# Kernel optimization log

Measured on AMD Instinct MI355X. Metric: run time of the kernel, lower is better.

## Reference

```python
import jax, jax.numpy as jnp
import numpy as np
import math

B, S, D, H, M = 2, 2048, 1024, 16, 64
HD = D // H  # head_dim = 64


def setup_inputs() -> dict:
    key = jax.random.key(0)
    ks = jax.random.split(key, 16)
    inp = {
        "query": jax.random.normal(ks[0], (B, S, D), jnp.float32),
        "key": jax.random.normal(ks[1], (B, S, D), jnp.float32),
        "value": jax.random.normal(ks[2], (B, S, D), jnp.float32),
        "mask": jax.random.randint(ks[3], (B, 1, 1, S), 0, 2, jnp.int32),
        "Wq": jax.random.normal(ks[4], (D, D), jnp.float32) * 0.02,
        "bq": jnp.zeros((D,), jnp.float32),
        "Wk": jax.random.normal(ks[5], (D, D), jnp.float32) * 0.02,
        "bk": jnp.zeros((D,), jnp.float32),
        "Wv": jax.random.normal(ks[6], (D, D), jnp.float32) * 0.02,
        "bv": jnp.zeros((D,), jnp.float32),
        "Wo": jax.random.normal(ks[7], (D, D), jnp.float32) * 0.02,
        "bo": jnp.zeros((D,), jnp.float32),
        "m_k": jax.random.normal(ks[8], (1, M, D), jnp.float32) * (1.0 / HD),
        "m_v": jax.random.normal(ks[9], (1, M, D), jnp.float32) * (1.0 / M),
    }
    return inp


def reference(query, key, value, mask, Wq, bq, Wk, bk, Wv, bv, Wo, bo, m_k, m_v):
    b, nq, d = query.shape
    nk = key.shape[1]
    h, hd, m = H, HD, M
    scale = math.sqrt(hd)

    Q = query @ Wq.T + bq                      # [b, nq, d]
    K = key @ Wk.T + bk                        # [b, nk, d]
    V = value @ Wv.T + bv                      # [b, nk, d]

    mk = scale * jnp.broadcast_to(m_k, (b, m, d))           # sqrt(head_dim)*m_k
    mv = math.sqrt(m) * jnp.broadcast_to(m_v, (b, m, d))    # sqrt(m)*m_v

    K = jnp.concatenate([K, mk], axis=1)       # [b, nk+m, d]
    V = jnp.concatenate([V, mv], axis=1)

    Qh = Q.reshape(b, nq, h, hd).transpose(0, 2, 1, 3)           # [b,h,nq,hd]
    Kh = K.reshape(b, nk + m, h, hd).transpose(0, 2, 1, 3)       # [b,h,nk+m,hd]
    Vh = V.reshape(b, nk + m, h, hd).transpose(0, 2, 1, 3)

    energy = jnp.einsum('bhqd,bhkd->bhqk', Qh, Kh) / scale       # [b,h,nq,nk+m]
    # mask only the first nk key columns; memory slots are never masked
    masked = jnp.where(mask == 0, jnp.float32(-1e20), energy[..., :nk])
    energy = jnp.concatenate([masked, energy[..., nk:]], axis=-1)

    attention = jax.nn.softmax(energy, axis=-1)
    x = jnp.einsum('bhqk,bhkd->bhqd', attention, Vh)             # [b,h,nq,hd]
    x = x.transpose(0, 2, 1, 3).reshape(b, nq, d)
    return x @ Wo.T + bo
```

## Files before the change

kernel.cpp:

```cpp
#include <hip/hip_runtime.h>
#include <hip/hip_bf16.h>
#include <stdint.h>

#define B_  2
#define S_  2048
#define D_  1024
#define H_  16
#define HD_ 64
#define M_  64
#define SKM (S_ + M_)
#define LOG2E 1.44269504088896340736f

typedef __attribute__((ext_vector_type(8))) short s16x8;
typedef __attribute__((ext_vector_type(4))) float f32x4;
typedef __attribute__((ext_vector_type(16))) float f32x16;

#define GLOAD16(gp, lp) __builtin_amdgcn_global_load_lds( \
    (const __attribute__((address_space(1))) void*)(gp),  \
    (__attribute__((address_space(3))) void*)(lp), 16, 0, 0)

#define WAITVM(N) do { asm volatile("s_waitcnt vmcnt(" #N ")" ::: "memory"); \
                       __builtin_amdgcn_sched_barrier(0); } while (0)
#define BARRIER() do { asm volatile("" ::: "memory"); \
                       __builtin_amdgcn_s_barrier(); \
                       asm volatile("" ::: "memory"); } while (0)

__device__ __forceinline__ unsigned short f2bf(float f) {
  union { float f; unsigned int u; } v; v.f = f;
  unsigned int r = v.u + 0x7fffu + ((v.u >> 16) & 1u);
  return (unsigned short)(r >> 16);
}

__device__ __forceinline__ unsigned pkbf(float lo, float hi) {
  union { __hip_bfloat162 b; unsigned u; } t;
  t.b = __float22bfloat162_rn(make_float2(lo, hi));
  return t.u;
}

__global__ void compact_mask(const int* __restrict__ mask,
                             int* __restrict__ idx, int* __restrict__ cnt) {
  const int b = blockIdx.x;
  __shared__ int base, wsum[4];
  if (threadIdx.x == 0) base = 0;
  const int lane = threadIdx.x & 63, w = threadIdx.x >> 6;
  __syncthreads();
  for (int c = 0; c < S_; c += 256) {
    int key = c + threadIdx.x;
    int mv = mask[b * S_ + key];
    unsigned long long bal = __ballot(mv != 0);
    int pre = __popcll(bal & ((1ull << lane) - 1ull));
    if (lane == 0) wsum[w] = __popcll(bal);
    __syncthreads();
    int woff = 0;
    for (int i = 0; i < w; i++) woff += wsum[i];
    int tot = wsum[0] + wsum[1] + wsum[2] + wsum[3];
    if (mv) idx[b * S_ + base + woff + pre] = key;
    __syncthreads();
    if (threadIdx.x == 0) base += tot;
    __syncthreads();
  }
  if (threadIdx.x == 0) cnt[b] = base;
}

__global__ void cvt_fused(const float* __restrict__ q,
                          const float* __restrict__ w0, const float* __restrict__ w1,
                          const float* __restrict__ w2, const float* __restrict__ w3,
                          const float* __restrict__ key, const float* __restrict__ value,
                          unsigned short* __restrict__ qf,
                          unsigned short* __restrict__ o0, unsigned short* __restrict__ o1,
                          unsigned short* __restrict__ o2, unsigned short* __restrict__ o3,
                          unsigned short* __restrict__ kf, unsigned short* __restrict__ vf,
                          const int* __restrict__ idx, const int* __restrict__ cnt) {
  const size_t NQs = (size_t)B_ * S_ * D_;
  if (blockIdx.x < 8192) {
    size_t i = ((size_t)blockIdx.x * 256 + threadIdx.x) * 4;
    const float* in; unsigned short* out; size_t off;
    if (i < NQs) { in = q; out = qf; off = i; }
    else {
      size_t j = i - NQs;
      int wsel = (int)(j >> 20);
      off = j & ((1u << 20) - 1);
      in  = (wsel == 0) ? w0 : (wsel == 1) ? w1 : (wsel == 2) ? w2 : w3;
      out = (wsel == 0) ? o0 : (wsel == 1) ? o1 : (wsel == 2) ? o2 : o3;
    }
    float4 v = *(const float4*)&in[off];
    ushort4 o;
    o.x = f2bf(v.x); o.y = f2bf(v.y); o.z = f2bf(v.z); o.w = f2bf(v.w);
    *(ushort4*)&out[off] = o;
  } else {
    int gid = blockIdx.x - 8192;
    int kv = gid >> 12, rem = gid & 4095;
    int b = rem >> 11, j = rem & 2047;
    if (j >= cnt[b]) return;
    const float* in = kv ? value : key;
    unsigned short* out = kv ? vf : kf;
    int src = idx[b * S_ + j];
    const float* ip = in + ((size_t)(b * S_) + src) * D_;
    unsigned short* op = out + ((size_t)(b * S_) + j) * D_;
    int t = threadIdx.x * 4;
    float4 v = *(const float4*)&ip[t];
    ushort4 o;
    o.x = f2bf(v.x); o.y = f2bf(v.y); o.z = f2bf(v.z); o.w = f2bf(v.w);
    *(ushort4*)&op[t] = o;
  }
}

__global__ void fill_mem(const float* __restrict__ mk, const float* __restrict__ mv,
                         unsigned short* __restrict__ Kb, unsigned short* __restrict__ VtG,
                         const int* __restrict__ cnt) {
  int i = blockIdx.x * 256 + threadIdx.x;
  int row = i >> 10, col = i & 1023;
  int hI = col >> 6, dd = col & 63;
  unsigned short kv = f2bf(8.0f * mk[i]);
  unsigned short vv = f2bf(8.0f * mv[i]);
#pragma unroll
  for (int b = 0; b < B_; b++) {
    int c = cnt[b];
    Kb[((size_t)(b * SKM) + c + row) * D_ + col] = kv;
    VtG[((size_t)(b * H_ + hI) * HD_ + dd) * SKM + c + row] = vv;
  }
}

__device__ __forceinline__ void gemm_core2(
    const unsigned short* __restrict__ A,
    const unsigned short* __restrict__ Bw,
    unsigned short* As, unsigned short* Bs,
    int mBase, int nBase, int K,
    int tid, f32x4 acc[4][2]) {
  const int lane = tid & 63, w = tid >> 6;
  const int wr = w >> 2, wc = w & 3;
  const int lr = lane & 15, lk = lane >> 4;
  const int srow = tid >> 2;
  const int cd = tid & 3;
  const int ca = cd ^ ((srow >> 1) & 3);
  const int NT = K / 32;

#define STAGE_(buf, k0)                                                          \
  {                                                                              \
    GLOAD16(&A[(size_t)(mBase + srow) * K + (k0) + ca * 8],                      \
            &As[(buf) * (128 * 32) + (w * 16) * 32]);                            \
    GLOAD16(&Bw[(size_t)(nBase + srow) * K + (k0) + ca * 8],                     \
            &Bs[(buf) * (128 * 32) + (w * 16) * 32]);                            \
  }

  STAGE_(0, 0);
  int cur = 0;
  for (int t = 0; t < NT; ++t) {
    if (t + 1 < NT) {
      STAGE_(cur ^ 1, (t + 1) * 32);
      WAITVM(2);
    } else {
      WAITVM(0);
    }
    BARRIER();
    s16x8 af[4], bf[2];
#pragma unroll
    for (int mi = 0; mi < 4; mi++) {
      int row = wr * 64 + mi * 16 + lr;
      af[mi] = *(const s16x8*)&As[cur * (128 * 32) + row * 32 + ((lk ^ ((row >> 1) & 3)) << 3)];
    }
#pragma unroll
    for (int ni = 0; ni < 2; ni++) {
      int row = wc * 32 + ni * 16 + lr;
      bf[ni] = *(const s16x8*)&Bs[cur * (128 * 32) + row * 32 + ((lk ^ ((row >> 1) & 3)) << 3)];
    }
#pragma unroll
    for (int mi = 0; mi < 4; mi++)
#pragma unroll
      for (int ni = 0; ni < 2; ni++)
        acc[mi][ni] = __builtin_amdgcn_mfma_f32_16x16x32_bf16(af[mi], bf[ni], acc[mi][ni], 0, 0, 0);
    BARRIER();
    cur ^= 1;
  }
#undef STAGE_
}

__global__ __launch_bounds__(512)
void gemm_qkv(const unsigned short* __restrict__ qf, const unsigned short* __restrict__ kf,
              const unsigned short* __restrict__ vf,
              const unsigned short* __restrict__ wq, const unsigned short* __restrict__ wk,
              const unsigned short* __restrict__ wv,
              const float* __restrict__ bq, const float* __restrict__ bk,
              const float* __restrict__ bv,
              unsigned short* __restrict__ Qb, unsigned short* __restrict__ Kb,
              unsigned short* __restrict__ Vt,
              const int* __restrict__ cnt) {
  __shared__ __align__(16) unsigned short As[2 * 128 * 32];
  __shared__ __align__(16) unsigned short Bs[2 * 128 * 32];
  const int z = blockIdx.x >> 8;
  const int local = blockIdx.x & 255;
  const int wsz = (local & 7) * 32 + (local >> 3);
  const int nBase = (wsz & 7) * 128, mBase = (wsz >> 3) * 128;
  const int bb = (mBase >= S_);
  if (z) {
    if (mBase - bb * S_ >= cnt[bb]) return;
  }
  const unsigned short* A  = (z == 0) ? qf : (z == 1) ? kf : vf;
  const unsigned short* Bw = (z == 0) ? wq : (z == 1) ? wk : wv;
  const float* bias        = (z == 0) ? bq : (z == 1) ? bk : bv;

  const int tid = threadIdx.x, lane = tid & 63;
  const int w = tid >> 6, wr = w >> 2, wc = w & 3;
  const int lr = lane & 15, lk = lane >> 4;

  const f32x4 fz = {0.f, 0.f, 0.f, 0.f};
  f32x4 acc[4][2];
#pragma unroll
  for (int i = 0; i < 4; i++)
#pragma unroll
    for (int j = 0; j < 2; j++) acc[i][j] = fz;

  gemm_core2(A, Bw, As, Bs, mBase, nBase, D_, tid, acc);

  const float alpha = (z == 0) ? 0.125f * LOG2E : 1.0f;
#pragma unroll
  for (int mi = 0; mi < 4; mi++)
#pragma unroll
    for (int ni = 0; ni < 2; ni++)
#pragma unroll
      for (int r = 0; r < 4; r++) {
        int gr = mBase + wr * 64 + mi * 16 + lk * 4 + r;
        int gc = nBase + wc * 32 + ni * 16 + lr;
        float v = (acc[mi][ni][r] + bias[gc]) * alpha;
        if (z == 2) {
          int s = gr - bb * S_;
          int hI = gc >> 6, dd = gc & 63;
          Vt[((size_t)(bb * H_ + hI) * HD_ + dd) * SKM + s] = f2bf(v);
        } else if (z == 1) {
          int orow = gr + bb * M_;
          Kb[(size_t)orow * D_ + gc] = f2bf(v);
        } else {
          Qb[(size_t)gr * D_ + gc] = f2bf(v);
        }
      }
}

__global__ __launch_bounds__(512)
void gemm_o(const unsigned short* __restrict__ A, const unsigned short* __restrict__ Bw,
            const float* __restrict__ bias, float* __restrict__ Cout) {
  __shared__ __align__(16) unsigned short As[2 * 128 * 32];
  __shared__ __align__(16) unsigned short Bs[2 * 128 * 32];
  const int local = blockIdx.x & 255;
  const int wsz = (local & 7) * 32 + (local >> 3);
  const int nBase = (wsz & 7) * 128, mBase = (wsz >> 3) * 128;
  const int tid = threadIdx.x, lane = tid & 63;
  const int w = tid >> 6, wr = w >> 2, wc = w & 3;
  const int lr = lane & 15, lk = lane >> 4;

  const f32x4 fz = {0.f, 0.f, 0.f, 0.f};
  f32x4 acc[4][2];
#pragma unroll
  for (int i = 0; i < 4; i++)
#pragma unroll
    for (int j = 0; j < 2; j++) acc[i][j] = fz;

  gemm_core2(A, Bw, As, Bs, mBase, nBase, D_, tid, acc);

#pragma unroll
  for (int mi = 0; mi < 4; mi++)
#pragma unroll
    for (int ni = 0; ni < 2; ni++)
#pragma unroll
      for (int r = 0; r < 4; r++) {
        int gr = mBase + wr * 64 + mi * 16 + lk * 4 + r;
        int gc = nBase + wc * 32 + ni * 16 + lr;
        Cout[(size_t)gr * D_ + gc] = acc[mi][ni][r] + bias[gc];
      }
}

__global__ __launch_bounds__(512)
void attn_kernel(const unsigned short* __restrict__ Qb,
                 const unsigned short* __restrict__ Kb,
                 const unsigned short* __restrict__ VtG,
                 const int* __restrict__ cnt,
                 unsigned short* __restrict__ Xb) {
  __shared__ __align__(16) unsigned short Ks[64 * 64];
  __shared__ __align__(16) unsigned short Vs[64 * 64];

  const int tid = threadIdx.x, lane = tid & 63, w = tid >> 6;
  const int l31 = lane & 31, hh = lane >> 5;
  const int qt = blockIdx.x, h = blockIdx.y, b = blockIdx.z;

  const int total = cnt[b] + M_;
  const int nt = (total + 63) >> 6;

  const int r0 = tid >> 3, c0 = tid & 7;
  const int ck = c0 ^ (r0 & 7);
  const unsigned short* Kg = Kb + (size_t)b * SKM * D_ + (size_t)h * HD_;
  const unsigned short* Vg = VtG + (size_t)(b * H_ + h) * HD_ * SKM;

  const unsigned short* qp = Qb + ((size_t)(b * S_) + qt * 256 + w * 32 + l31) * D_ + h * HD_;
  s16x8 qf[4];
#pragma unroll
  for (int ds = 0; ds < 4; ds++) qf[ds] = *(const s16x8*)&qp[ds * 16 + hh * 8];

  f32x16 accO[2];
#pragma unroll
  for (int dt = 0; dt < 2; dt++)
#pragma unroll
    for (int j = 0; j < 16; j++) accO[dt][j] = 0.f;
  float m_r = -1e20f, l_r = 0.f;

  uint4 kr0, vr0;
  auto LOAD = [&](int kt) {
    kr0 = *(const uint4*)&Kg[(size_t)(kt * 64 + r0) * D_ + c0 * 8];
    vr0 = *(const uint4*)&Vg[(size_t)r0 * SKM + kt * 64 + c0 * 8];
  };
  LOAD(0);

  for (int kt = 0; kt < nt; ++kt) {
    __syncthreads();
    *(uint4*)&Ks[r0 * 64 + ck * 8] = kr0;
    *(uint4*)&Vs[r0 * 64 + ck * 8] = vr0;
    __syncthreads();
    if (kt + 1 < nt) LOAD(kt + 1);

    f32x16 p0, p1;
#pragma unroll
    for (int j = 0; j < 16; j++) { p0[j] = 0.f; p1[j] = 0.f; }
    __builtin_amdgcn_s_setprio(1);
#pragma unroll
    for (int ds = 0; ds < 4; ds++) {
      s16x8 ka0 = *(const s16x8*)&Ks[l31 * 64 + (((ds * 2 + hh) ^ (l31 & 7)) << 3)];
      s16x8 ka1 = *(const s16x8*)&Ks[(32 + l31) * 64 + (((ds * 2 + hh) ^ (l31 & 7)) << 3)];
      p0 = __builtin_amdgcn_mfma_f32_32x32x16_bf16(ka0, qf[ds], p0, 0, 0, 0);
      p1 = __builtin_amdgcn_mfma_f32_32x32x16_bf16(ka1, qf[ds], p1, 0, 0, 0);
    }
    __builtin_amdgcn_s_setprio(0);

    if (kt == nt - 1) {
      int valid = total - kt * 64;
#pragma unroll
      for (int j = 0; j < 16; j++) {
        int kl = (j & 3) + 8 * (j >> 2) + 4 * hh;
        if (kl >= valid) p0[j] = -1e30f;
        if (kl + 32 >= valid) p1[j] = -1e30f;
      }
    }

    float vmax = fmaxf(p0[0], p1[0]);
#pragma unroll
    for (int j = 1; j < 16; j++) vmax = fmaxf(vmax, fmaxf(p0[j], p1[j]));
    vmax = fmaxf(vmax, __shfl_xor(vmax, 32));
    if (!__all(vmax - m_r <= 8.0f)) {
      float mnew = fmaxf(m_r, vmax);
      float fac = __builtin_amdgcn_exp2f(m_r - mnew);
      m_r = mnew;
      l_r *= fac;
#pragma unroll
      for (int dt = 0; dt < 2; dt++)
#pragma unroll
        for (int j = 0; j < 16; j++) accO[dt][j] *= fac;
    }
    float sum = 0.f;
#pragma unroll
    for (int j = 0; j < 16; j++) {
      p0[j] = __builtin_amdgcn_exp2f(p0[j] - m_r); sum += p0[j];
      p1[j] = __builtin_amdgcn_exp2f(p1[j] - m_r); sum += p1[j];
    }
    sum += __shfl_xor(sum, 32);
    l_r += sum;

    s16x8 pf_[4];
#pragma unroll
    for (int ks = 0; ks < 4; ks++) {
      const int base = (ks & 1) * 8;
#define ELT(t) ((ks >= 2) ? p1[base + (t)] : p0[base + (t)])
      unsigned w0 = pkbf(ELT(0), ELT(1));
      unsigned w1 = pkbf(ELT(2), ELT(3));
      unsigned w2 = pkbf(ELT(4), ELT(5));
      unsigned w3 = pkbf(ELT(6), ELT(7));
#undef ELT
      unsigned s0 = hh ? w0 : w2;
      unsigned s1 = hh ? w1 : w3;
      unsigned g0 = (unsigned)__shfl_xor((int)s0, 32);
      unsigned g1 = (unsigned)__shfl_xor((int)s1, 32);
      union { s16x8 v; unsigned u[4]; } pf;
      pf.u[0] = hh ? g0 : w0;
      pf.u[1] = hh ? g1 : w1;
      pf.u[2] = hh ? w2 : g0;
      pf.u[3] = hh ? w3 : g1;
      pf_[ks] = pf.v;
    }

    __builtin_amdgcn_s_setprio(1);
#pragma unroll
    for (int dt = 0; dt < 2; dt++)
#pragma unroll
      for (int ks = 0; ks < 4; ks++) {
        s16x8 va = *(const s16x8*)&Vs[(dt * 32 + l31) * 64 + (((ks * 2 + hh) ^ (l31 & 7)) << 3)];
        accO[dt] = __builtin_amdgcn_mfma_f32_32x32x16_bf16(va, pf_[ks], accO[dt], 0, 0, 0);
      }
    __builtin_amdgcn_s_setprio(0);
  }

  float invl = 1.0f / l_r;
  size_t orow = ((size_t)(b * S_) + qt * 256 + w * 32 + l31) * D_ + h * HD_;
#pragma unroll
  for (int dt = 0; dt < 2; dt++)
#pragma unroll
    for (int j = 0; j < 16; j++) {
      int d = dt * 32 + (j & 3) + 8 * (j >> 2) + 4 * hh;
      Xb[orow + d] = f2bf(accO[dt][j] * invl);
    }
}

extern "C" void kernel_launch(void* const* d_in, const int* in_sizes, int n_in,
                              void* d_out, int out_size, void* d_ws, size_t ws_size,
                              hipStream_t stream) {
  const float* query = (const float*)d_in[0];
  const float* key   = (const float*)d_in[1];
  const float* value = (const float*)d_in[2];
  const int*   mask  = (const int*)d_in[3];
  const float* Wq    = (const float*)d_in[4];
  const float* bq    = (const float*)d_in[5];
  const float* Wk    = (const float*)d_in[6];
  const float* bk    = (const float*)d_in[7];
  const float* Wv    = (const float*)d_in[8];
  const float* bv    = (const float*)d_in[9];
  const float* Wo    = (const float*)d_in[10];
  const float* bo    = (const float*)d_in[11];
  const float* m_k   = (const float*)d_in[12];
  const float* m_v   = (const float*)d_in[13];

  const int NQ = B_ * S_ * D_;
  const int NW = D_ * D_;
  const int NK = B_ * SKM * D_;

  unsigned short* ws = (unsigned short*)d_ws;
  unsigned short* qf = ws;
  unsigned short* kf = qf + NQ;
  unsigned short* vf = kf + NQ;
  unsigned short* wq = vf + NQ;
  unsigned short* wk = wq + NW;
  unsigned short* wv = wk + NW;
  unsigned short* wo = wv + NW;
  unsigned short* Qb = wo + NW;
  unsigned short* Kb = Qb + NQ;
  unsigned short* Vt = Kb + NK;
  unsigned short* Xb = Vt + NK;
  int* idx = (int*)(Xb + NQ);
  int* cnt = idx + B_ * S_;

  compact_mask<<<B_, 256, 0, stream>>>(mask, idx, cnt);
  cvt_fused<<<16384, 256, 0, stream>>>(query, Wq, Wk, Wv, Wo, key, value,
                                       qf, wq, wk, wv, wo, kf, vf, idx, cnt);

  gemm_qkv<<<768, 512, 0, stream>>>(qf, kf, vf, wq, wk, wv, bq, bk, bv, Qb, Kb, Vt, cnt);
  fill_mem<<<(M_ * D_) / 256, 256, 0, stream>>>(m_k, m_v, Kb, Vt, cnt);

  attn_kernel<<<dim3(S_ / 256, H_, B_), 512, 0, stream>>>(Qb, Kb, Vt, cnt, Xb);

  gemm_o<<<256, 512, 0, stream>>>(Xb, wo, bo, (float*)d_out);
}
```

Measured before the change: 125.0 us.

## Enlarge GEMM tiles to K=64 with 1024-thread blocks for QKV and output projections

Replaces the shared GEMM core with inlined per-kernel loops that stage 64-wide K slices, halving the number of barrier-separated iterations, and use an 8-way XOR swizzle. The QKV GEMM moves to 256x128 output tiles with 16 waves, so each block has more data reuse and fewer blocks are launched. The output GEMM keeps 128x128 tiles but spreads them over 16 waves with smaller per-wave accumulators. In exchange, each block uses more LDS and there are fewer blocks for the QKV launch, which can hurt occupancy and load balance on 256 CUs.

New measurement: 128.4 us. 1.03x slower.

```diff
diff --git a/kernel.cpp b/kernel.cpp
--- a/kernel.cpp
+++ b/kernel.cpp
@@ -121,61 +121,7 @@
   }
 }
 
-__device__ __forceinline__ void gemm_core2(
-    const unsigned short* __restrict__ A,
-    const unsigned short* __restrict__ Bw,
-    unsigned short* As, unsigned short* Bs,
-    int mBase, int nBase, int K,
-    int tid, f32x4 acc[4][2]) {
-  const int lane = tid & 63, w = tid >> 6;
-  const int wr = w >> 2, wc = w & 3;
-  const int lr = lane & 15, lk = lane >> 4;
-  const int srow = tid >> 2;
-  const int cd = tid & 3;
-  const int ca = cd ^ ((srow >> 1) & 3);
-  const int NT = K / 32;
-
-#define STAGE_(buf, k0)                                                          \
-  {                                                                              \
-    GLOAD16(&A[(size_t)(mBase + srow) * K + (k0) + ca * 8],                      \
-            &As[(buf) * (128 * 32) + (w * 16) * 32]);                            \
-    GLOAD16(&Bw[(size_t)(nBase + srow) * K + (k0) + ca * 8],                     \
-            &Bs[(buf) * (128 * 32) + (w * 16) * 32]);                            \
-  }
-
-  STAGE_(0, 0);
-  int cur = 0;
-  for (int t = 0; t < NT; ++t) {
-    if (t + 1 < NT) {
-      STAGE_(cur ^ 1, (t + 1) * 32);
-      WAITVM(2);
-    } else {
-      WAITVM(0);
-    }
-    BARRIER();
-    s16x8 af[4], bf[2];
-#pragma unroll
-    for (int mi = 0; mi < 4; mi++) {
-      int row = wr * 64 + mi * 16 + lr;
-      af[mi] = *(const s16x8*)&As[cur * (128 * 32) + row * 32 + ((lk ^ ((row >> 1) & 3)) << 3)];
-    }
-#pragma unroll
-    for (int ni = 0; ni < 2; ni++) {
-      int row = wc * 32 + ni * 16 + lr;
-      bf[ni] = *(const s16x8*)&Bs[cur * (128 * 32) + row * 32 + ((lk ^ ((row >> 1) & 3)) << 3)];
-    }
-#pragma unroll
-    for (int mi = 0; mi < 4; mi++)
-#pragma unroll
-      for (int ni = 0; ni < 2; ni++)
-        acc[mi][ni] = __builtin_amdgcn_mfma_f32_16x16x32_bf16(af[mi], bf[ni], acc[mi][ni], 0, 0, 0);
-    BARRIER();
-    cur ^= 1;
-  }
-#undef STAGE_
-}
-
-__global__ __launch_bounds__(512)
+__global__ __launch_bounds__(1024)
 void gemm_qkv(const unsigned short* __restrict__ qf, const unsigned short* __restrict__ kf,
               const unsigned short* __restrict__ vf,
               const unsigned short* __restrict__ wq, const unsigned short* __restrict__ wk,
@@ -185,12 +131,12 @@
               unsigned short* __restrict__ Qb, unsigned short* __restrict__ Kb,
               unsigned short* __restrict__ Vt,
               const int* __restrict__ cnt) {
-  __shared__ __align__(16) unsigned short As[2 * 128 * 32];
-  __shared__ __align__(16) unsigned short Bs[2 * 128 * 32];
-  const int z = blockIdx.x >> 8;
-  const int local = blockIdx.x & 255;
-  const int wsz = (local & 7) * 32 + (local >> 3);
-  const int nBase = (wsz & 7) * 128, mBase = (wsz >> 3) * 128;
+  __shared__ __align__(16) unsigned short As[2 * 256 * 64];
+  __shared__ __align__(16) unsigned short Bs[2 * 128 * 64];
+  const int z = blockIdx.x >> 7;
+  const int local = blockIdx.x & 127;
+  const int wsz = (local & 7) * 16 + (local >> 3);
+  const int nBase = (wsz & 7) * 128, mBase = (wsz >> 3) * 256;
   const int bb = (mBase >= S_);
   if (z) {
     if (mBase - bb * S_ >= cnt[bb]) return;
@@ -200,8 +146,11 @@
   const float* bias        = (z == 0) ? bq : (z == 1) ? bk : bv;
 
   const int tid = threadIdx.x, lane = tid & 63;
-  const int w = tid >> 6, wr = w >> 2, wc = w & 3;
+  const int w = tid >> 6;
+  const int wr = w >> 2, wc = w & 3;
   const int lr = lane & 15, lk = lane >> 4;
+  const int sr = w * 8 + (lane >> 3);
+  const int ca = (lane & 7) ^ (sr & 7);
 
   const f32x4 fz = {0.f, 0.f, 0.f, 0.f};
   f32x4 acc[4][2];
@@ -210,7 +159,51 @@
 #pragma unroll
     for (int j = 0; j < 2; j++) acc[i][j] = fz;
 
-  gemm_core2(A, Bw, As, Bs, mBase, nBase, D_, tid, acc);
+  const int NT = D_ / 64;
+
+#define STAGE_(buf, k0)                                                           \
+  {                                                                               \
+    GLOAD16(&A[(size_t)(mBase + sr) * D_ + (k0) + ca * 8],                        \
+            &As[(buf) * (256 * 64) + (w * 8) * 64]);                              \
+    GLOAD16(&A[(size_t)(mBase + 128 + sr) * D_ + (k0) + ca * 8],                  \
+            &As[(buf) * (256 * 64) + (128 + w * 8) * 64]);                        \
+    GLOAD16(&Bw[(size_t)(nBase + sr) * D_ + (k0) + ca * 8],                       \
+            &Bs[(buf) * (128 * 64) + (w * 8) * 64]);                              \
+  }
+
+  STAGE_(0, 0);
+  int cur = 0;
+  for (int t = 0; t < NT; ++t) {
+    if (t + 1 < NT) {
+      STAGE_(cur ^ 1, (t + 1) * 64);
+      WAITVM(3);
+    } else {
+      WAITVM(0);
+    }
+    BARRIER();
+#pragma unroll
+    for (int ks = 0; ks < 2; ks++) {
+      s16x8 af[4], bf[2];
+#pragma unroll
+      for (int mi = 0; mi < 4; mi++) {
+        int row = wr * 64 + mi * 16 + lr;
+        af[mi] = *(const s16x8*)&As[cur * (256 * 64) + row * 64 + (((ks * 4 + lk) ^ (row & 7)) << 3)];
+      }
+#pragma unroll
+      for (int ni = 0; ni < 2; ni++) {
+        int row = wc * 32 + ni * 16 + lr;
+        bf[ni] = *(const s16x8*)&Bs[cur * (128 * 64) + row * 64 + (((ks * 4 + lk) ^ (row & 7)) << 3)];
+      }
+#pragma unroll
+      for (int mi = 0; mi < 4; mi++)
+#pragma unroll
+        for (int ni = 0; ni < 2; ni++)
+          acc[mi][ni] = __builtin_amdgcn_mfma_f32_16x16x32_bf16(af[mi], bf[ni], acc[mi][ni], 0, 0, 0);
+    }
+    BARRIER();
+    cur ^= 1;
+  }
+#undef STAGE_
 
   const float alpha = (z == 0) ? 0.125f * LOG2E : 1.0f;
 #pragma unroll
@@ -235,34 +228,79 @@
       }
 }
 
-__global__ __launch_bounds__(512)
+__global__ __launch_bounds__(1024)
 void gemm_o(const unsigned short* __restrict__ A, const unsigned short* __restrict__ Bw,
             const float* __restrict__ bias, float* __restrict__ Cout) {
-  __shared__ __align__(16) unsigned short As[2 * 128 * 32];
-  __shared__ __align__(16) unsigned short Bs[2 * 128 * 32];
-  const int local = blockIdx.x & 255;
+  __shared__ __align__(16) unsigned short As[2 * 128 * 64];
+  __shared__ __align__(16) unsigned short Bs[2 * 128 * 64];
+  const int local = blockIdx.x;
   const int wsz = (local & 7) * 32 + (local >> 3);
   const int nBase = (wsz & 7) * 128, mBase = (wsz >> 3) * 128;
   const int tid = threadIdx.x, lane = tid & 63;
-  const int w = tid >> 6, wr = w >> 2, wc = w & 3;
+  const int w = tid >> 6;
+  const int wr = w >> 2, wc = w & 3;
   const int lr = lane & 15, lk = lane >> 4;
+  const int sr = w * 8 + (lane >> 3);
+  const int ca = (lane & 7) ^ (sr & 7);
 
   const f32x4 fz = {0.f, 0.f, 0.f, 0.f};
-  f32x4 acc[4][2];
-#pragma unroll
-  for (int i = 0; i < 4; i++)
+  f32x4 acc[2][2];
+#pragma unroll
+  for (int i = 0; i < 2; i++)
 #pragma unroll
     for (int j = 0; j < 2; j++) acc[i][j] = fz;
 
-  gemm_core2(A, Bw, As, Bs, mBase, nBase, D_, tid, acc);
-
-#pragma unroll
-  for (int mi = 0; mi < 4; mi++)
+  const int NT = D_ / 64;
+
+#define STAGE_(buf, k0)                                                           \
+  {                                                                               \
+    GLOAD16(&A[(size_t)(mBase + sr) * D_ + (k0) + ca * 8],                        \
+            &As[(buf) * (128 * 64) + (w * 8) * 64]);                              \
+    GLOAD16(&Bw[(size_t)(nBase + sr) * D_ + (k0) + ca * 8],                       \
+            &Bs[(buf) * (128 * 64) + (w * 8) * 64]);                              \
+  }
+
+  STAGE_(0, 0);
+  int cur = 0;
+  for (int t = 0; t < NT; ++t) {
+    if (t + 1 < NT) {
+      STAGE_(cur ^ 1, (t + 1) * 64);
+      WAITVM(2);
+    } else {
+      WAITVM(0);
+    }
+    BARRIER();
+#pragma unroll
+    for (int ks = 0; ks < 2; ks++) {
+      s16x8 af[2], bf[2];
+#pragma unroll
+      for (int mi = 0; mi < 2; mi++) {
+        int row = wr * 32 + mi * 16 + lr;
+        af[mi] = *(const s16x8*)&As[cur * (128 * 64) + row * 64 + (((ks * 4 + lk) ^ (row & 7)) << 3)];
+      }
+#pragma unroll
+      for (int ni = 0; ni < 2; ni++) {
+        int row = wc * 32 + ni * 16 + lr;
+        bf[ni] = *(const s16x8*)&Bs[cur * (128 * 64) + row * 64 + (((ks * 4 + lk) ^ (row & 7)) << 3)];
+      }
+#pragma unroll
+      for (int mi = 0; mi < 2; mi++)
+#pragma unroll
+        for (int ni = 0; ni < 2; ni++)
+          acc[mi][ni] = __builtin_amdgcn_mfma_f32_16x16x32_bf16(af[mi], bf[ni], acc[mi][ni], 0, 0, 0);
+    }
+    BARRIER();
+    cur ^= 1;
+  }
+#undef STAGE_
+
+#pragma unroll
+  for (int mi = 0; mi < 2; mi++)
 #pragma unroll
     for (int ni = 0; ni < 2; ni++)
 #pragma unroll
       for (int r = 0; r < 4; r++) {
-        int gr = mBase + wr * 64 + mi * 16 + lk * 4 + r;
+        int gr = mBase + wr * 32 + mi * 16 + lk * 4 + r;
         int gc = nBase + wc * 32 + ni * 16 + lr;
         Cout[(size_t)gr * D_ + gc] = acc[mi][ni][r] + bias[gc];
       }
@@ -446,10 +484,10 @@
   cvt_fused<<<16384, 256, 0, stream>>>(query, Wq, Wk, Wv, Wo, key, value,
                                        qf, wq, wk, wv, wo, kf, vf, idx, cnt);
 
-  gemm_qkv<<<768, 512, 0, stream>>>(qf, kf, vf, wq, wk, wv, bq, bk, bv, Qb, Kb, Vt, cnt);
+  gemm_qkv<<<384, 1024, 0, stream>>>(qf, kf, vf, wq, wk, wv, bq, bk, bv, Qb, Kb, Vt, cnt);
   fill_mem<<<(M_ * D_) / 256, 256, 0, stream>>>(m_k, m_v, Kb, Vt, cnt);
 
   attn_kernel<<<dim3(S_ / 256, H_, B_), 512, 0, stream>>>(Qb, Kb, Vt, cnt, Xb);
 
-  gemm_o<<<256, 512, 0, stream>>>(Xb, wo, bo, (float*)d_out);
-}
+  gemm_o<<<256, 1024, 0, stream>>>(Xb, wo, bo, (float*)d_out);
+}
```

## Widen GEMM K-tile to 64 and double-buffer attention K/V in LDS

Applied to the files above, without the earlier changes.

The shared GEMM core now stages 64-wide K slices instead of 32, using four async global-to-LDS loads per stage with a new XOR swizzle, which halves the number of barrier-separated iterations. The attention kernel double-buffers its K and V tiles in LDS: the next tile is written into the alternate buffer after compute, so each iteration needs one barrier instead of two. The cost is twice the LDS per block in both GEMMs and in attention, which may reduce occupancy.

After: 122.9 us. About the same (-1.7%).

```diff
diff --git a/kernel.cpp b/kernel.cpp
--- a/kernel.cpp
+++ b/kernel.cpp
@@ -121,54 +121,61 @@
   }
 }
 
-__device__ __forceinline__ void gemm_core2(
+__device__ __forceinline__ void gemm_core64(
     const unsigned short* __restrict__ A,
     const unsigned short* __restrict__ Bw,
     unsigned short* As, unsigned short* Bs,
-    int mBase, int nBase, int K,
+    int mBase, int nBase,
     int tid, f32x4 acc[4][2]) {
   const int lane = tid & 63, w = tid >> 6;
   const int wr = w >> 2, wc = w & 3;
   const int lr = lane & 15, lk = lane >> 4;
-  const int srow = tid >> 2;
-  const int cd = tid & 3;
-  const int ca = cd ^ ((srow >> 1) & 3);
-  const int NT = K / 32;
+  const int rg = lane >> 3;
+  const int sr0 = w * 8 + rg;
+  const int ca = (lane & 7) ^ (rg & 7);
+  const int NT = D_ / 64;
 
 #define STAGE_(buf, k0)                                                          \
   {                                                                              \
-    GLOAD16(&A[(size_t)(mBase + srow) * K + (k0) + ca * 8],                      \
-            &As[(buf) * (128 * 32) + (w * 16) * 32]);                            \
-    GLOAD16(&Bw[(size_t)(nBase + srow) * K + (k0) + ca * 8],                     \
-            &Bs[(buf) * (128 * 32) + (w * 16) * 32]);                            \
+    GLOAD16(&A[(size_t)(mBase + sr0) * D_ + (k0) + ca * 8],                      \
+            &As[(buf) * (128 * 64) + (w * 8) * 64]);                             \
+    GLOAD16(&A[(size_t)(mBase + 64 + sr0) * D_ + (k0) + ca * 8],                 \
+            &As[(buf) * (128 * 64) + (64 + w * 8) * 64]);                        \
+    GLOAD16(&Bw[(size_t)(nBase + sr0) * D_ + (k0) + ca * 8],                     \
+            &Bs[(buf) * (128 * 64) + (w * 8) * 64]);                             \
+    GLOAD16(&Bw[(size_t)(nBase + 64 + sr0) * D_ + (k0) + ca * 8],                \
+            &Bs[(buf) * (128 * 64) + (64 + w * 8) * 64]);                        \
   }
 
   STAGE_(0, 0);
   int cur = 0;
   for (int t = 0; t < NT; ++t) {
     if (t + 1 < NT) {
-      STAGE_(cur ^ 1, (t + 1) * 32);
-      WAITVM(2);
+      STAGE_(cur ^ 1, (t + 1) * 64);
+      WAITVM(4);
     } else {
       WAITVM(0);
     }
     BARRIER();
-    s16x8 af[4], bf[2];
-#pragma unroll
-    for (int mi = 0; mi < 4; mi++) {
-      int row = wr * 64 + mi * 16 + lr;
-      af[mi] = *(const s16x8*)&As[cur * (128 * 32) + row * 32 + ((lk ^ ((row >> 1) & 3)) << 3)];
-    }
-#pragma unroll
-    for (int ni = 0; ni < 2; ni++) {
-      int row = wc * 32 + ni * 16 + lr;
-      bf[ni] = *(const s16x8*)&Bs[cur * (128 * 32) + row * 32 + ((lk ^ ((row >> 1) & 3)) << 3)];
-    }
-#pragma unroll
-    for (int mi = 0; mi < 4; mi++)
-#pragma unroll
-      for (int ni = 0; ni < 2; ni++)
-        acc[mi][ni] = __builtin_amdgcn_mfma_f32_16x16x32_bf16(af[mi], bf[ni], acc[mi][ni], 0, 0, 0);
+#pragma unroll
+    for (int ks = 0; ks < 2; ks++) {
+      s16x8 af[4], bf[2];
+#pragma unroll
+      for (int mi = 0; mi < 4; mi++) {
+        int row = wr * 64 + mi * 16 + lr;
+        af[mi] = *(const s16x8*)&As[cur * (128 * 64) + row * 64 + (((ks * 4 + lk) ^ (row & 7)) << 3)];
+      }
+#pragma unroll
+      for (int ni = 0; ni < 2; ni++) {
+        int row = wc * 32 + ni * 16 + lr;
+        bf[ni] = *(const s16x8*)&Bs[cur * (128 * 64) + row * 64 + (((ks * 4 + lk) ^ (row & 7)) << 3)];
+      }
+#pragma unroll
+      for (int mi = 0; mi < 4; mi++)
+#pragma unroll
+        for (int ni = 0; ni < 2; ni++)
+          acc[mi][ni] = __builtin_amdgcn_mfma_f32_16x16x32_bf16(af[mi], bf[ni], acc[mi][ni], 0, 0, 0);
+    }
     BARRIER();
     cur ^= 1;
   }
@@ -185,8 +192,8 @@
               unsigned short* __restrict__ Qb, unsigned short* __restrict__ Kb,
               unsigned short* __restrict__ Vt,
               const int* __restrict__ cnt) {
-  __shared__ __align__(16) unsigned short As[2 * 128 * 32];
-  __shared__ __align__(16) unsigned short Bs[2 * 128 * 32];
+  __shared__ __align__(16) unsigned short As[2 * 128 * 64];
+  __shared__ __align__(16) unsigned short Bs[2 * 128 * 64];
   const int z = blockIdx.x >> 8;
   const int local = blockIdx.x & 255;
   const int wsz = (local & 7) * 32 + (local >> 3);
@@ -210,7 +217,7 @@
 #pragma unroll
     for (int j = 0; j < 2; j++) acc[i][j] = fz;
 
-  gemm_core2(A, Bw, As, Bs, mBase, nBase, D_, tid, acc);
+  gemm_core64(A, Bw, As, Bs, mBase, nBase, tid, acc);
 
   const float alpha = (z == 0) ? 0.125f * LOG2E : 1.0f;
 #pragma unroll
@@ -238,8 +245,8 @@
 __global__ __launch_bounds__(512)
 void gemm_o(const unsigned short* __restrict__ A, const unsigned short* __restrict__ Bw,
             const float* __restrict__ bias, float* __restrict__ Cout) {
-  __shared__ __align__(16) unsigned short As[2 * 128 * 32];
-  __shared__ __align__(16) unsigned short Bs[2 * 128 * 32];
+  __shared__ __align__(16) unsigned short As[2 * 128 * 64];
+  __shared__ __align__(16) unsigned short Bs[2 * 128 * 64];
   const int local = blockIdx.x & 255;
   const int wsz = (local & 7) * 32 + (local >> 3);
   const int nBase = (wsz & 7) * 128, mBase = (wsz >> 3) * 128;
@@ -254,7 +261,7 @@
 #pragma unroll
     for (int j = 0; j < 2; j++) acc[i][j] = fz;
 
-  gemm_core2(A, Bw, As, Bs, mBase, nBase, D_, tid, acc);
+  gemm_core64(A, Bw, As, Bs, mBase, nBase, tid, acc);
 
 #pragma unroll
   for (int mi = 0; mi < 4; mi++)
@@ -274,8 +281,8 @@
                  const unsigned short* __restrict__ VtG,
                  const int* __restrict__ cnt,
                  unsigned short* __restrict__ Xb) {
-  __shared__ __align__(16) unsigned short Ks[64 * 64];
-  __shared__ __align__(16) unsigned short Vs[64 * 64];
+  __shared__ __align__(16) unsigned short Ks[2 * 64 * 64];
+  __shared__ __align__(16) unsigned short Vs[2 * 64 * 64];
 
   const int tid = threadIdx.x, lane = tid & 63, w = tid >> 6;
   const int l31 = lane & 31, hh = lane >> 5;
@@ -306,23 +313,27 @@
     kr0 = *(const uint4*)&Kg[(size_t)(kt * 64 + r0) * D_ + c0 * 8];
     vr0 = *(const uint4*)&Vg[(size_t)r0 * SKM + kt * 64 + c0 * 8];
   };
+
   LOAD(0);
+  *(uint4*)&Ks[r0 * 64 + ck * 8] = kr0;
+  *(uint4*)&Vs[r0 * 64 + ck * 8] = vr0;
+  __syncthreads();
+  int cur = 0;
 
   for (int kt = 0; kt < nt; ++kt) {
-    __syncthreads();
-    *(uint4*)&Ks[r0 * 64 + ck * 8] = kr0;
-    *(uint4*)&Vs[r0 * 64 + ck * 8] = vr0;
-    __syncthreads();
-    if (kt + 1 < nt) LOAD(kt + 1);
-
+    const bool pre = (kt + 1 < nt);
+    if (pre) LOAD(kt + 1);
+
+    const unsigned short* Kc = &Ks[cur * 4096];
+    const unsigned short* Vc = &Vs[cur * 4096];
     f32x16 p0, p1;
 #pragma unroll
     for (int j = 0; j < 16; j++) { p0[j] = 0.f; p1[j] = 0.f; }
     __builtin_amdgcn_s_setprio(1);
 #pragma unroll
     for (int ds = 0; ds < 4; ds++) {
-      s16x8 ka0 = *(const s16x8*)&Ks[l31 * 64 + (((ds * 2 + hh) ^ (l31 & 7)) << 3)];
-      s16x8 ka1 = *(const s16x8*)&Ks[(32 + l31) * 64 + (((ds * 2 + hh) ^ (l31 & 7)) << 3)];
+      s16x8 ka0 = *(const s16x8*)&Kc[l31 * 64 + (((ds * 2 + hh) ^ (l31 & 7)) << 3)];
+      s16x8 ka1 = *(const s16x8*)&Kc[(32 + l31) * 64 + (((ds * 2 + hh) ^ (l31 & 7)) << 3)];
       p0 = __builtin_amdgcn_mfma_f32_32x32x16_bf16(ka0, qf[ds], p0, 0, 0, 0);
       p1 = __builtin_amdgcn_mfma_f32_32x32x16_bf16(ka1, qf[ds], p1, 0, 0, 0);
     }
@@ -388,10 +399,17 @@
     for (int dt = 0; dt < 2; dt++)
 #pragma unroll
       for (int ks = 0; ks < 4; ks++) {
-        s16x8 va = *(const s16x8*)&Vs[(dt * 32 + l31) * 64 + (((ks * 2 + hh) ^ (l31 & 7)) << 3)];
+        s16x8 va = *(const s16x8*)&Vc[(dt * 32 + l31) * 64 + (((ks * 2 + hh) ^ (l31 & 7)) << 3)];
         accO[dt] = __builtin_amdgcn_mfma_f32_32x32x16_bf16(va, pf_[ks], accO[dt], 0, 0, 0);
       }
     __builtin_amdgcn_s_setprio(0);
+
+    if (pre) {
+      *(uint4*)&Ks[(cur ^ 1) * 4096 + r0 * 64 + ck * 8] = kr0;
+      *(uint4*)&Vs[(cur ^ 1) * 4096 + r0 * 64 + ck * 8] = vr0;
+      __syncthreads();
+      cur ^= 1;
+    }
   }
 
   float invl = 1.0f / l_r;
```
